# Kernel optimization log

Measured on AMD Instinct MI355X. Metric: run time of the kernel, lower is better.

## Reference

```python
import jax, jax.numpy as jnp
import numpy as np

N = 65536          # rays per batch
NC = 64            # coarse samples (config.num_samples_coarse)
NF = 128           # fine samples (config.num_samples_fine)
NEAR, FAR = 0.1, 1000.0


def setup_inputs() -> dict:
    key = jax.random.key(0)
    k = jax.random.split(key, 7)
    ray_origins = jax.random.normal(k[0], (N, 3), jnp.float32)
    ray_directions = jax.random.normal(k[1], (N, 3), jnp.float32)
    # stratified coarse t_vals == sample_points_along_rays(stratified=True)
    t = NEAR + (FAR - NEAR) * jnp.linspace(0.0, 1.0, NC, dtype=jnp.float32)
    t = jnp.broadcast_to(t, (N, NC))
    mids = 0.5 * (t[:, 1:] + t[:, :-1])
    upper = jnp.concatenate([mids, t[:, -1:]], axis=-1)
    lower = jnp.concatenate([t[:, :1], mids], axis=-1)
    t_rand = jax.random.uniform(k[2], (N, NC), jnp.float32)
    coarse_t_vals = lower + (upper - lower) * t_rand
    coarse_weights = jax.random.uniform(k[3], (N, NC), jnp.float32)
    u = jax.random.uniform(k[4], (N, NF), jnp.float32)
    colors = jax.random.uniform(k[5], (N, NC + NF, 3), jnp.float32)
    densities = jax.random.uniform(k[6], (N, NC + NF, 1), jnp.float32)
    return {"ray_origins": ray_origins, "ray_directions": ray_directions,
            "coarse_weights": coarse_weights, "coarse_t_vals": coarse_t_vals,
            "u": u, "colors": colors, "densities": densities}


def _hierarchical_sampling(ray_origins, ray_directions, coarse_weights, coarse_t_vals, u):
    # inverse-CDF importance resampling (GridNeRFRenderer.hierarchical_sampling)
    w = coarse_weights + 1e-5
    pdf = w / jnp.sum(w, axis=-1, keepdims=True)                 # [N, NC]
    cdf = jnp.cumsum(pdf, axis=-1)
    cdf = jnp.concatenate([jnp.zeros_like(cdf[..., :1]), cdf], axis=-1)  # [N, NC+1]
    # per-ray searchsorted (right)
    indices = jax.vmap(lambda c, uu: jnp.searchsorted(c, uu, side="right"))(cdf, u)  # [N, NF]
    nc = coarse_t_vals.shape[-1]
    below = jnp.clip(indices - 1, 0, nc - 1)
    above = jnp.clip(indices, 0, nc - 1)
    cdf_b = jnp.take_along_axis(cdf, below, axis=1)
    cdf_a = jnp.take_along_axis(cdf, above, axis=1)
    t_b = jnp.take_along_axis(coarse_t_vals, below, axis=1)
    t_a = jnp.take_along_axis(coarse_t_vals, above, axis=1)
    denom = cdf_a - cdf_b
    denom = jnp.where(denom < 1e-5, jnp.ones_like(denom), denom)
    tt = (u - cdf_b) / denom
    fine_t_vals = t_b + tt * (t_a - t_b)
    combined_t_vals = jnp.sort(jnp.concatenate([coarse_t_vals, fine_t_vals], axis=-1), axis=-1)  # [N, NC+NF]
    fine_points = ray_origins[:, None, :] + ray_directions[:, None, :] * combined_t_vals[..., None]
    return fine_points, combined_t_vals


def _volume_rendering(colors, densities, t_vals, ray_directions):
    dists = t_vals[..., 1:] - t_vals[..., :-1]
    dists = jnp.concatenate([dists, jnp.full_like(dists[..., :1], 1e10)], axis=-1)
    dists = dists * jnp.linalg.norm(ray_directions, axis=-1, keepdims=True)   # [N, S]
    alpha = 1.0 - jnp.exp(-densities[..., 0] * dists)                         # [N, S]
    # exclusive cumprod transmittance (== cumprod + roll + T[...,0]=1)
    trans = jnp.cumprod(1.0 - alpha + 1e-10, axis=-1)
    trans = jnp.concatenate([jnp.ones_like(trans[..., :1]), trans[..., :-1]], axis=-1)
    weights = alpha * trans
    rgb = jnp.sum(weights[..., None] * colors, axis=-2)   # [N, 3]
    depth = jnp.sum(weights * t_vals, axis=-1)            # [N]
    opacity = jnp.sum(weights, axis=-1)                   # [N]
    return rgb, depth, opacity, weights


def reference(ray_origins, ray_directions, coarse_weights, coarse_t_vals, u, colors, densities):
    fine_points, combined_t_vals = _hierarchical_sampling(
        ray_origins, ray_directions, coarse_weights, coarse_t_vals, u)
    rgb, depth, opacity, weights = _volume_rendering(
        colors, densities, combined_t_vals, ray_directions)
    return (rgb, depth, opacity, fine_points)
```

## Files before the change

kernel.cpp:

```cpp
#include <hip/hip_runtime.h>
#include <math.h>


#define NRAYS 65536
#define NCC   64
#define NFF   128
#define SS    192

__global__ __launch_bounds__(256)
void nerf_fused(const float* __restrict__ ro,  const float* __restrict__ rd,
                const float* __restrict__ cw,  const float* __restrict__ ct,
                const float* __restrict__ uu,  const float* __restrict__ col,
                const float* __restrict__ den, float* __restrict__ out)
{
    const int lane = threadIdx.x & 63;
    const int wv   = threadIdx.x >> 6;
    const int ray  = blockIdx.x * 4 + wv;

    __shared__ float s_cdf[4][65];
    __shared__ float s_ct [4][64];
    __shared__ float s_su [4][128];
    __shared__ float s_vals[4][256];

    float wt = cw[(size_t)ray * NCC + lane] + 1e-5f;
    float tc = ct[(size_t)ray * NCC + lane];
    float x = wt;
    #pragma unroll
    for (int off = 1; off < 64; off <<= 1) {
        float y = __shfl_up(x, off);
        if (lane >= off) x += y;
    }
    float total = __shfl(x, 63);
    float cv = x / total;
    #pragma unroll
    for (int off = 1; off < 64; off <<= 1) {
        float y = __shfl_up(cv, off);
        if (lane >= off) cv = fmaxf(cv, y);
    }
    s_cdf[wv][lane + 1] = cv;
    if (lane == 0) s_cdf[wv][0] = 0.0f;
    s_ct[wv][lane] = tc;

    float2 u2 = *(const float2*)(uu + (size_t)ray * NFF + 2 * lane);
    float v0 = u2.x, v1 = u2.y;
    #pragma unroll
    for (int k = 2; k <= 128; k <<= 1) {
        #pragma unroll
        for (int j = k >> 1; j >= 1; j >>= 1) {
            bool up = (((lane << 1) & k) == 0);
            if (j == 1) {
                float a = v0, b = v1;
                v0 = up ? fminf(a, b) : fmaxf(a, b);
                v1 = up ? fmaxf(a, b) : fminf(a, b);
            } else {
                int m = j >> 1;
                bool keepmin = (((lane & m) == 0) == up);
                float p0 = __shfl_xor(v0, m);
                float p1 = __shfl_xor(v1, m);
                v0 = keepmin ? fminf(v0, p0) : fmaxf(v0, p0);
                v1 = keepmin ? fminf(v1, p1) : fmaxf(v1, p1);
            }
        }
    }
    *(float2*)&s_su[wv][2 * lane] = make_float2(v0, v1);

    const float* cdfp = s_cdf[wv];
    const float* ctp  = s_ct[wv];
    float us[2] = {v0, v1};
    #pragma unroll
    for (int q = 0; q < 2; ++q) {
        float u = us[q];
        int pos = 0;
        #pragma unroll
        for (int st = 32; st >= 1; st >>= 1) {
            int np = pos + st;
            pos = (cdfp[np] <= u) ? np : pos;
        }
        int above = (pos + 1 < 63) ? (pos + 1) : 63;
        float cb = cdfp[pos], ca = cdfp[above];
        float tb = ctp[pos],  ta = ctp[above];
        float dnm = ca - cb;
        dnm = (dnm < 1e-5f) ? 1.0f : dnm;
        float tt = (u - cb) / dnm;
        float fval = tb + tt * (ta - tb);
        int rank = 2 * lane + q + pos + 1;
        s_vals[wv][rank] = fval;
    }

    const float* sup = s_su[wv];
    float key = cdfp[lane];
    int cnt = 0;
    #pragma unroll
    for (int st = 128; st >= 1; st >>= 1) {
        int np = cnt + st;
        bool ok = (np <= 128) && (sup[np - 1] < key);
        cnt = ok ? np : cnt;
    }
    s_vals[wv][lane + cnt] = tc;
    s_vals[wv][192 + lane] = 0.0f;

    float4 sv = *(const float4*)&s_vals[wv][4 * lane];
    float v[4] = {sv.x, sv.y, sv.z, sv.w};

    float dx = rd[(size_t)ray * 3 + 0], dy = rd[(size_t)ray * 3 + 1], dz = rd[(size_t)ray * 3 + 2];
    float ox = ro[(size_t)ray * 3 + 0], oy = ro[(size_t)ray * 3 + 1], oz = ro[(size_t)ray * 3 + 2];
    float nrm = sqrtf(dx * dx + dy * dy + dz * dz);

    const bool active = lane < 48;
    float tnext = __shfl_down(v[0], 1);
    float dd[4];
    dd[0] = v[1] - v[0];
    dd[1] = v[2] - v[1];
    dd[2] = v[3] - v[2];
    dd[3] = (lane == 47) ? 1e10f : (tnext - v[3]);

    float4 dn4 = make_float4(0.f, 0.f, 0.f, 0.f);
    if (active) dn4 = *(const float4*)(den + (size_t)ray * SS + 4 * lane);
    float dnv[4] = {dn4.x, dn4.y, dn4.z, dn4.w};

    float aa[4], ff[4];
    #pragma unroll
    for (int r = 0; r < 4; ++r) {
        float al = active ? (1.0f - expf(-dnv[r] * (dd[r] * nrm))) : 0.0f;
        aa[r] = al;
        ff[r] = active ? (1.0f - al + 1e-10f) : 1.0f;
    }

    if (active) {
        float* fp = out + (size_t)5 * NRAYS + (size_t)ray * (SS * 3) + 12 * lane;
        float4 p0 = make_float4(ox + dx * v[0], oy + dy * v[0], oz + dz * v[0], ox + dx * v[1]);
        float4 p1 = make_float4(oy + dy * v[1], oz + dz * v[1], ox + dx * v[2], oy + dy * v[2]);
        float4 p2 = make_float4(oz + dz * v[2], ox + dx * v[3], oy + dy * v[3], oz + dz * v[3]);
        *(float4*)(fp + 0) = p0;
        *(float4*)(fp + 4) = p1;
        *(float4*)(fp + 8) = p2;
    }

    float pr1 = ff[0], pr2 = ff[0] * ff[1], pr3 = pr2 * ff[2];
    float sx = pr3 * ff[3];
    #pragma unroll
    for (int off = 1; off < 64; off <<= 1) {
        float y = __shfl_up(sx, off);
        if (lane >= off) sx *= y;
    }
    float excl = __shfl_up(sx, 1);
    if (lane == 0) excl = 1.0f;
    float w0 = aa[0] * excl;
    float w1 = aa[1] * (excl * pr1);
    float w2 = aa[2] * (excl * pr2);
    float w3 = aa[3] * (excl * pr3);

    float4 c0 = make_float4(0.f,0.f,0.f,0.f), c1 = c0, c2 = c0;
    if (active) {
        const float* cp = col + (size_t)ray * (SS * 3) + 12 * lane;
        c0 = *(const float4*)(cp + 0);
        c1 = *(const float4*)(cp + 4);
        c2 = *(const float4*)(cp + 8);
    }
    float rr  = w0 * c0.x + w1 * c0.w + w2 * c1.z + w3 * c2.y;
    float gg  = w0 * c0.y + w1 * c1.x + w2 * c1.w + w3 * c2.z;
    float bb  = w0 * c0.z + w1 * c1.y + w2 * c2.x + w3 * c2.w;
    float dep = w0 * v[0] + w1 * v[1] + w2 * v[2] + w3 * v[3];
    float opa = w0 + w1 + w2 + w3;

    #pragma unroll
    for (int off = 32; off >= 1; off >>= 1) {
        rr  += __shfl_xor(rr,  off);
        gg  += __shfl_xor(gg,  off);
        bb  += __shfl_xor(bb,  off);
        dep += __shfl_xor(dep, off);
        opa += __shfl_xor(opa, off);
    }
    if (lane == 0) {
        out[(size_t)ray * 3 + 0] = rr;
        out[(size_t)ray * 3 + 1] = gg;
        out[(size_t)ray * 3 + 2] = bb;
        out[(size_t)3 * NRAYS + ray] = dep;
        out[(size_t)4 * NRAYS + ray] = opa;
    }
}

extern "C" void kernel_launch(void* const* d_in, const int* in_sizes, int n_in,
                              void* d_out, int out_size, void* d_ws, size_t ws_size,
                              hipStream_t stream) {
    const float* ro  = (const float*)d_in[0];
    const float* rd  = (const float*)d_in[1];
    const float* cw  = (const float*)d_in[2];
    const float* ct  = (const float*)d_in[3];
    const float* uu  = (const float*)d_in[4];
    const float* col = (const float*)d_in[5];
    const float* den = (const float*)d_in[6];
    float* out = (float*)d_out;
    (void)in_sizes; (void)n_in; (void)out_size; (void)d_ws; (void)ws_size;
    nerf_fused<<<NRAYS / 4, 256, 0, stream>>>(ro, rd, cw, ct, uu, col, den, out);
}
```

Before: 344.9 us.

## Process two rays per wavefront, histogram-based merge ranks, drop cdf max-scan

Each wavefront now handles two rays, interleaving their prefix scans, bitonic sorts and searches so the independent shuffle chains can overlap and hide latency. The binary search over sorted u values that placed the coarse t samples is replaced by an LDS atomic histogram of search positions followed by a prefix scan. The running-max monotonicity scan on the CDF is removed, and launch bounds now request higher occupancy. Costs are higher register pressure from two rays per wave and LDS atomics. Dropping the max-scan relies on the cumulative sum being monotone in float arithmetic.

```diff
diff --git a/kernel.cpp b/kernel.cpp
--- a/kernel.cpp
+++ b/kernel.cpp
@@ -7,7 +7,7 @@
 #define NFF   128
 #define SS    192
 
-__global__ __launch_bounds__(256)
+__global__ __launch_bounds__(256, 6)
 void nerf_fused(const float* __restrict__ ro,  const float* __restrict__ rd,
                 const float* __restrict__ cw,  const float* __restrict__ ct,
                 const float* __restrict__ uu,  const float* __restrict__ col,
@@ -15,168 +15,195 @@
 {
     const int lane = threadIdx.x & 63;
     const int wv   = threadIdx.x >> 6;
-    const int ray  = blockIdx.x * 4 + wv;
-
-    __shared__ float s_cdf[4][65];
-    __shared__ float s_ct [4][64];
-    __shared__ float s_su [4][128];
-    __shared__ float s_vals[4][256];
-
-    float wt = cw[(size_t)ray * NCC + lane] + 1e-5f;
-    float tc = ct[(size_t)ray * NCC + lane];
-    float x = wt;
+    const int ray0 = blockIdx.x * 8 + wv * 2;
+    const int sl0  = wv * 2;
+
+    __shared__ float s_cdf [8][65];
+    __shared__ float s_ct  [8][64];
+    __shared__ float s_vals[8][256];
+    __shared__ int   s_hist[8][64];
+
+    float wt[2], tc[2];
+    float2 u2[2];
+    #pragma unroll
+    for (int r = 0; r < 2; ++r) {
+        const size_t ray = ray0 + r;
+        wt[r] = cw[ray * NCC + lane] + 1e-5f;
+        tc[r] = ct[ray * NCC + lane];
+        u2[r] = *(const float2*)(uu + ray * NFF + 2 * lane);
+        s_hist[sl0 + r][lane] = 0;
+    }
+
+    float x0 = wt[0], x1 = wt[1];
     #pragma unroll
     for (int off = 1; off < 64; off <<= 1) {
-        float y = __shfl_up(x, off);
-        if (lane >= off) x += y;
-    }
-    float total = __shfl(x, 63);
-    float cv = x / total;
-    #pragma unroll
-    for (int off = 1; off < 64; off <<= 1) {
-        float y = __shfl_up(cv, off);
-        if (lane >= off) cv = fmaxf(cv, y);
-    }
-    s_cdf[wv][lane + 1] = cv;
-    if (lane == 0) s_cdf[wv][0] = 0.0f;
-    s_ct[wv][lane] = tc;
-
-    float2 u2 = *(const float2*)(uu + (size_t)ray * NFF + 2 * lane);
-    float v0 = u2.x, v1 = u2.y;
+        float y0 = __shfl_up(x0, off);
+        float y1 = __shfl_up(x1, off);
+        if (lane >= off) { x0 += y0; x1 += y1; }
+    }
+    float t0 = __shfl(x0, 63), t1 = __shfl(x1, 63);
+    s_cdf[sl0][lane + 1]     = x0 / t0;
+    s_cdf[sl0 + 1][lane + 1] = x1 / t1;
+    if (lane == 0) { s_cdf[sl0][0] = 0.0f; s_cdf[sl0 + 1][0] = 0.0f; }
+    s_ct[sl0][lane]     = tc[0];
+    s_ct[sl0 + 1][lane] = tc[1];
+
+    float a0 = u2[0].x, a1 = u2[0].y;
+    float b0 = u2[1].x, b1 = u2[1].y;
     #pragma unroll
     for (int k = 2; k <= 128; k <<= 1) {
         #pragma unroll
         for (int j = k >> 1; j >= 1; j >>= 1) {
             bool up = (((lane << 1) & k) == 0);
             if (j == 1) {
-                float a = v0, b = v1;
-                v0 = up ? fminf(a, b) : fmaxf(a, b);
-                v1 = up ? fmaxf(a, b) : fminf(a, b);
+                float m0 = fminf(a0, a1), M0 = fmaxf(a0, a1);
+                float m1 = fminf(b0, b1), M1 = fmaxf(b0, b1);
+                a0 = up ? m0 : M0;  a1 = up ? M0 : m0;
+                b0 = up ? m1 : M1;  b1 = up ? M1 : m1;
             } else {
-                int m = j >> 1;
+                const int m = j >> 1;
                 bool keepmin = (((lane & m) == 0) == up);
-                float p0 = __shfl_xor(v0, m);
-                float p1 = __shfl_xor(v1, m);
-                v0 = keepmin ? fminf(v0, p0) : fmaxf(v0, p0);
-                v1 = keepmin ? fminf(v1, p1) : fmaxf(v1, p1);
+                float pa0 = __shfl_xor(a0, m), pa1 = __shfl_xor(a1, m);
+                float pb0 = __shfl_xor(b0, m), pb1 = __shfl_xor(b1, m);
+                a0 = keepmin ? fminf(a0, pa0) : fmaxf(a0, pa0);
+                a1 = keepmin ? fminf(a1, pa1) : fmaxf(a1, pa1);
+                b0 = keepmin ? fminf(b0, pb0) : fmaxf(b0, pb0);
+                b1 = keepmin ? fminf(b1, pb1) : fmaxf(b1, pb1);
             }
         }
     }
-    *(float2*)&s_su[wv][2 * lane] = make_float2(v0, v1);
-
-    const float* cdfp = s_cdf[wv];
-    const float* ctp  = s_ct[wv];
-    float us[2] = {v0, v1};
-    #pragma unroll
-    for (int q = 0; q < 2; ++q) {
-        float u = us[q];
-        int pos = 0;
-        #pragma unroll
-        for (int st = 32; st >= 1; st >>= 1) {
-            int np = pos + st;
-            pos = (cdfp[np] <= u) ? np : pos;
-        }
-        int above = (pos + 1 < 63) ? (pos + 1) : 63;
-        float cb = cdfp[pos], ca = cdfp[above];
-        float tb = ctp[pos],  ta = ctp[above];
-        float dnm = ca - cb;
-        dnm = (dnm < 1e-5f) ? 1.0f : dnm;
-        float tt = (u - cb) / dnm;
-        float fval = tb + tt * (ta - tb);
-        int rank = 2 * lane + q + pos + 1;
-        s_vals[wv][rank] = fval;
-    }
-
-    const float* sup = s_su[wv];
-    float key = cdfp[lane];
-    int cnt = 0;
-    #pragma unroll
-    for (int st = 128; st >= 1; st >>= 1) {
-        int np = cnt + st;
-        bool ok = (np <= 128) && (sup[np - 1] < key);
-        cnt = ok ? np : cnt;
-    }
-    s_vals[wv][lane + cnt] = tc;
-    s_vals[wv][192 + lane] = 0.0f;
-
-    float4 sv = *(const float4*)&s_vals[wv][4 * lane];
-    float v[4] = {sv.x, sv.y, sv.z, sv.w};
-
-    float dx = rd[(size_t)ray * 3 + 0], dy = rd[(size_t)ray * 3 + 1], dz = rd[(size_t)ray * 3 + 2];
-    float ox = ro[(size_t)ray * 3 + 0], oy = ro[(size_t)ray * 3 + 1], oz = ro[(size_t)ray * 3 + 2];
-    float nrm = sqrtf(dx * dx + dy * dy + dz * dz);
-
-    const bool active = lane < 48;
-    float tnext = __shfl_down(v[0], 1);
-    float dd[4];
-    dd[0] = v[1] - v[0];
-    dd[1] = v[2] - v[1];
-    dd[2] = v[3] - v[2];
-    dd[3] = (lane == 47) ? 1e10f : (tnext - v[3]);
-
-    float4 dn4 = make_float4(0.f, 0.f, 0.f, 0.f);
-    if (active) dn4 = *(const float4*)(den + (size_t)ray * SS + 4 * lane);
-    float dnv[4] = {dn4.x, dn4.y, dn4.z, dn4.w};
-
-    float aa[4], ff[4];
-    #pragma unroll
-    for (int r = 0; r < 4; ++r) {
-        float al = active ? (1.0f - expf(-dnv[r] * (dd[r] * nrm))) : 0.0f;
-        aa[r] = al;
-        ff[r] = active ? (1.0f - al + 1e-10f) : 1.0f;
-    }
-
-    if (active) {
-        float* fp = out + (size_t)5 * NRAYS + (size_t)ray * (SS * 3) + 12 * lane;
-        float4 p0 = make_float4(ox + dx * v[0], oy + dy * v[0], oz + dz * v[0], ox + dx * v[1]);
-        float4 p1 = make_float4(oy + dy * v[1], oz + dz * v[1], ox + dx * v[2], oy + dy * v[2]);
-        float4 p2 = make_float4(oz + dz * v[2], ox + dx * v[3], oy + dy * v[3], oz + dz * v[3]);
-        *(float4*)(fp + 0) = p0;
-        *(float4*)(fp + 4) = p1;
-        *(float4*)(fp + 8) = p2;
-    }
-
-    float pr1 = ff[0], pr2 = ff[0] * ff[1], pr3 = pr2 * ff[2];
-    float sx = pr3 * ff[3];
+
+    #pragma unroll
+    for (int r = 0; r < 2; ++r) {
+        const int sl = sl0 + r;
+        const float* cdfp = s_cdf[sl];
+        const float* ctp  = s_ct[sl];
+        float us[2];
+        us[0] = r ? b0 : a0;
+        us[1] = r ? b1 : a1;
+        #pragma unroll
+        for (int q = 0; q < 2; ++q) {
+            float u = us[q];
+            int pos = 0; float cb = 0.0f;
+            #pragma unroll
+            for (int st = 32; st >= 1; st >>= 1) {
+                int np = pos + st;
+                float cv = cdfp[np];
+                bool ok = (cv <= u);
+                pos = ok ? np : pos;
+                cb  = ok ? cv : cb;
+            }
+            int above = (pos + 1 < 63) ? (pos + 1) : 63;
+            float ca = cdfp[above];
+            float tb = ctp[pos], ta = ctp[above];
+            float dnm = ca - cb;
+            dnm = (dnm < 1e-5f) ? 1.0f : dnm;
+            float fval = tb + ((u - cb) / dnm) * (ta - tb);
+            s_vals[sl][2 * lane + q + pos + 1] = fval;
+            atomicAdd(&s_hist[sl][pos], 1);
+        }
+    }
+
+    int h0 = s_hist[sl0][lane];
+    int h1 = s_hist[sl0 + 1][lane];
+    int i0 = h0, i1 = h1;
     #pragma unroll
     for (int off = 1; off < 64; off <<= 1) {
-        float y = __shfl_up(sx, off);
-        if (lane >= off) sx *= y;
-    }
-    float excl = __shfl_up(sx, 1);
-    if (lane == 0) excl = 1.0f;
-    float w0 = aa[0] * excl;
-    float w1 = aa[1] * (excl * pr1);
-    float w2 = aa[2] * (excl * pr2);
-    float w3 = aa[3] * (excl * pr3);
-
-    float4 c0 = make_float4(0.f,0.f,0.f,0.f), c1 = c0, c2 = c0;
-    if (active) {
-        const float* cp = col + (size_t)ray * (SS * 3) + 12 * lane;
-        c0 = *(const float4*)(cp + 0);
-        c1 = *(const float4*)(cp + 4);
-        c2 = *(const float4*)(cp + 8);
-    }
-    float rr  = w0 * c0.x + w1 * c0.w + w2 * c1.z + w3 * c2.y;
-    float gg  = w0 * c0.y + w1 * c1.x + w2 * c1.w + w3 * c2.z;
-    float bb  = w0 * c0.z + w1 * c1.y + w2 * c2.x + w3 * c2.w;
-    float dep = w0 * v[0] + w1 * v[1] + w2 * v[2] + w3 * v[3];
-    float opa = w0 + w1 + w2 + w3;
-
-    #pragma unroll
-    for (int off = 32; off >= 1; off >>= 1) {
-        rr  += __shfl_xor(rr,  off);
-        gg  += __shfl_xor(gg,  off);
-        bb  += __shfl_xor(bb,  off);
-        dep += __shfl_xor(dep, off);
-        opa += __shfl_xor(opa, off);
-    }
-    if (lane == 0) {
-        out[(size_t)ray * 3 + 0] = rr;
-        out[(size_t)ray * 3 + 1] = gg;
-        out[(size_t)ray * 3 + 2] = bb;
-        out[(size_t)3 * NRAYS + ray] = dep;
-        out[(size_t)4 * NRAYS + ray] = opa;
+        int y0 = __shfl_up(i0, off);
+        int y1 = __shfl_up(i1, off);
+        if (lane >= off) { i0 += y0; i1 += y1; }
+    }
+    int c0 = __shfl_up(i0, 1), c1 = __shfl_up(i1, 1);
+    if (lane == 0) { c0 = 0; c1 = 0; }
+    s_vals[sl0][lane + c0]     = tc[0];
+    s_vals[sl0 + 1][lane + c1] = tc[1];
+    s_vals[sl0][192 + lane]     = 0.0f;
+    s_vals[sl0 + 1][192 + lane] = 0.0f;
+
+    #pragma unroll
+    for (int r = 0; r < 2; ++r) {
+        const int sl = sl0 + r;
+        const size_t ray = ray0 + r;
+
+        float4 sv = *(const float4*)&s_vals[sl][4 * lane];
+        float v[4] = {sv.x, sv.y, sv.z, sv.w};
+
+        float dx = rd[ray * 3 + 0], dy = rd[ray * 3 + 1], dz = rd[ray * 3 + 2];
+        float ox = ro[ray * 3 + 0], oy = ro[ray * 3 + 1], oz = ro[ray * 3 + 2];
+        float nrm = sqrtf(dx * dx + dy * dy + dz * dz);
+
+        const bool active = lane < 48;
+        float tnext = __shfl_down(v[0], 1);
+        float dd[4];
+        dd[0] = v[1] - v[0];
+        dd[1] = v[2] - v[1];
+        dd[2] = v[3] - v[2];
+        dd[3] = (lane == 47) ? 1e10f : (tnext - v[3]);
+
+        float4 dn4 = make_float4(0.f, 0.f, 0.f, 0.f);
+        if (active) dn4 = *(const float4*)(den + ray * SS + 4 * lane);
+        float dnv[4] = {dn4.x, dn4.y, dn4.z, dn4.w};
+
+        float aa[4], ff[4];
+        #pragma unroll
+        for (int s = 0; s < 4; ++s) {
+            float al = active ? (1.0f - expf(-dnv[s] * (dd[s] * nrm))) : 0.0f;
+            aa[s] = al;
+            ff[s] = active ? (1.0f - al + 1e-10f) : 1.0f;
+        }
+
+        if (active) {
+            float* fp = out + (size_t)5 * NRAYS + ray * (SS * 3) + 12 * lane;
+            float4 p0 = make_float4(ox + dx * v[0], oy + dy * v[0], oz + dz * v[0], ox + dx * v[1]);
+            float4 p1 = make_float4(oy + dy * v[1], oz + dz * v[1], ox + dx * v[2], oy + dy * v[2]);
+            float4 p2 = make_float4(oz + dz * v[2], ox + dx * v[3], oy + dy * v[3], oz + dz * v[3]);
+            *(float4*)(fp + 0) = p0;
+            *(float4*)(fp + 4) = p1;
+            *(float4*)(fp + 8) = p2;
+        }
+
+        float pr1 = ff[0], pr2 = ff[0] * ff[1], pr3 = pr2 * ff[2];
+        float sx = pr3 * ff[3];
+        #pragma unroll
+        for (int off = 1; off < 64; off <<= 1) {
+            float y = __shfl_up(sx, off);
+            if (lane >= off) sx *= y;
+        }
+        float excl = __shfl_up(sx, 1);
+        if (lane == 0) excl = 1.0f;
+        float w0 = aa[0] * excl;
+        float w1 = aa[1] * (excl * pr1);
+        float w2 = aa[2] * (excl * pr2);
+        float w3 = aa[3] * (excl * pr3);
+
+        float4 cc0 = make_float4(0.f,0.f,0.f,0.f), cc1 = cc0, cc2 = cc0;
+        if (active) {
+            const float* cp = col + ray * (SS * 3) + 12 * lane;
+            cc0 = *(const float4*)(cp + 0);
+            cc1 = *(const float4*)(cp + 4);
+            cc2 = *(const float4*)(cp + 8);
+        }
+        float rr  = w0 * cc0.x + w1 * cc0.w + w2 * cc1.z + w3 * cc2.y;
+        float gg  = w0 * cc0.y + w1 * cc1.x + w2 * cc1.w + w3 * cc2.z;
+        float bb  = w0 * cc0.z + w1 * cc1.y + w2 * cc2.x + w3 * cc2.w;
+        float dep = w0 * v[0] + w1 * v[1] + w2 * v[2] + w3 * v[3];
+        float opa = w0 + w1 + w2 + w3;
+
+        #pragma unroll
+        for (int off = 32; off >= 1; off >>= 1) {
+            rr  += __shfl_xor(rr,  off);
+            gg  += __shfl_xor(gg,  off);
+            bb  += __shfl_xor(bb,  off);
+            dep += __shfl_xor(dep, off);
+            opa += __shfl_xor(opa, off);
+        }
+        if (lane == 0) {
+            out[ray * 3 + 0] = rr;
+            out[ray * 3 + 1] = gg;
+            out[ray * 3 + 2] = bb;
+            out[(size_t)3 * NRAYS + ray] = dep;
+            out[(size_t)4 * NRAYS + ray] = opa;
+        }
     }
 }
 
@@ -192,5 +219,5 @@
     const float* den = (const float*)d_in[6];
     float* out = (float*)d_out;
     (void)in_sizes; (void)n_in; (void)out_size; (void)d_ws; (void)ws_size;
-    nerf_fused<<<NRAYS / 4, 256, 0, stream>>>(ro, rd, cw, ct, uu, col, den, out);
+    nerf_fused<<<NRAYS / 8, 256, 0, stream>>>(ro, rd, cw, ct, uu, col, den, out);
 }
```

Measured after the change: 349.9 us. Within noise of the previous version (+1.4%).
